# Kernel tuning notes

Measured on AMD Instinct MI355X. Metric: run time of the kernel, lower is better.

## Reference

```python
import jax, jax.numpy as jnp
import numpy as np


def setup_inputs() -> dict:
    key = jax.random.key(0)
    k1, _ = jax.random.split(key)
    x = jax.random.normal(k1, (32, 64, 192, 192), dtype=jnp.float32)
    gamma = jnp.zeros((1,), dtype=jnp.float32)
    return {"x": x, "gamma": gamma}


def reference(x, gamma):
    B, C, H, W = x.shape
    q = x.reshape(B, C, H * W)                      # [B, C, N]
    # energy[b, c, d] = <q[b,c,:], q[b,d,:]>
    energy = jnp.einsum('bcn,bdn->bcd', q, q)       # [B, C, C]
    # max-subtract trick: softmax over (max - energy)
    energy_new = jnp.max(energy, axis=-1, keepdims=True) - energy
    attention = jax.nn.softmax(energy_new, axis=-1)  # [B, C, C]
    out = jnp.einsum('bcd,bdn->bcn', attention, q)   # [B, C, N]
    out = out.reshape(B, C, H, W)
    return x * (gamma[0] * out) + x
```

## Files before the change

### kernel.cpp

```cpp
#include <hip/hip_runtime.h>


#define BATCH 32
#define CH 64
#define NSP 36864

#define KSPLIT 32
#define KPER (NSP / KSPLIT)
#define BK 128
#define SITER (KPER / BK)

#define NB 128
#define NCHUNK 4
#define NBLKY (NSP / (NB * NCHUNK))
#define XSTR 132

using frag  = __attribute__((ext_vector_type(8))) short;
using f32x4 = __attribute__((ext_vector_type(4))) float;

__device__ inline unsigned short f2bf(float f) {
    unsigned u = __builtin_bit_cast(unsigned, f);
    unsigned r = (u + 0x7FFFu + ((u >> 16) & 1u)) >> 16;
    return (unsigned short)r;
}
__device__ inline unsigned pack2(float a, float b) {
    return (unsigned)f2bf(a) | ((unsigned)f2bf(b) << 16);
}
__device__ inline int rotn(int c, int n) {
    return (n + (((c >> 3) & 3) << 4)) & (NB - 1);
}

__global__ __launch_bounds__(256, 4) void gram_kernel(const float* __restrict__ x,
                                                      float* __restrict__ part) {
    const int b = blockIdx.x;
    const int kb = blockIdx.y;
    const int tid = threadIdx.x;
    const int wv = tid >> 6;
    const int lane = tid & 63;
    const int l15 = lane & 15;
    const int quad = lane >> 4;

    __shared__ unsigned short tile[2][CH][BK + 8];

    const float* xb = x + (size_t)b * CH * NSP + (size_t)kb * KPER;

    f32x4 acc[4];
#pragma unroll
    for (int cb = 0; cb < 4; cb++)
#pragma unroll
        for (int r = 0; r < 4; r++) acc[cb][r] = 0.f;

    float4 v[8];
#pragma unroll
    for (int rep = 0; rep < 8; rep++) {
        int idx = rep * 256 + tid;
        int c = idx >> 5, kq = idx & 31;
        v[rep] = *(const float4*)&xb[(size_t)c * NSP + kq * 4];
    }

    int p = 0;
    for (int s = 0; s < SITER; s++) {
#pragma unroll
        for (int rep = 0; rep < 8; rep++) {
            int idx = rep * 256 + tid;
            int c = idx >> 5, kq = idx & 31;
            uint2 pp;
            pp.x = pack2(v[rep].x, v[rep].y);
            pp.y = pack2(v[rep].z, v[rep].w);
            *(uint2*)&tile[p][c][kq * 4] = pp;
        }
        __syncthreads();
        if (s + 1 < SITER) {
#pragma unroll
            for (int rep = 0; rep < 8; rep++) {
                int idx = rep * 256 + tid;
                int c = idx >> 5, kq = idx & 31;
                v[rep] = *(const float4*)&xb[(size_t)c * NSP + (s + 1) * BK + kq * 4];
            }
        }
#pragma unroll
        for (int ks = 0; ks < 4; ks++) {
            frag a = *(const frag*)&tile[p][wv * 16 + l15][ks * 32 + quad * 8];
#pragma unroll
            for (int cb = 0; cb < 4; cb++) {
                frag bb = *(const frag*)&tile[p][cb * 16 + l15][ks * 32 + quad * 8];
                acc[cb] = __builtin_amdgcn_mfma_f32_16x16x32_bf16(a, bb, acc[cb], 0, 0, 0);
            }
        }
        p ^= 1;
    }

    float* eb = part + ((size_t)kb * BATCH + b) * CH * CH;
#pragma unroll
    for (int cb = 0; cb < 4; cb++)
#pragma unroll
        for (int r = 0; r < 4; r++) {
            int row = wv * 16 + quad * 4 + r;
            int col = cb * 16 + l15;
            eb[row * CH + col] = acc[cb][r];
        }
}

__global__ __launch_bounds__(64) void softmax_kernel(const float* __restrict__ part,
                                                     float* __restrict__ att) {
    const int row = blockIdx.x;
    const int d = threadIdx.x;

    float e = 0.f;
#pragma unroll
    for (int kb = 0; kb < KSPLIT; kb++)
        e += part[(size_t)kb * (BATCH * CH * CH) + (size_t)row * CH + d];

    float m = e;
#pragma unroll
    for (int off = 32; off > 0; off >>= 1) m = fmaxf(m, __shfl_down(m, off));
    m = __shfl(m, 0);

    float en = m - e;

    float mx = en;
#pragma unroll
    for (int off = 32; off > 0; off >>= 1) mx = fmaxf(mx, __shfl_down(mx, off));
    mx = __shfl(mx, 0);

    float ex = __expf(en - mx);
    float s = ex;
#pragma unroll
    for (int off = 32; off > 0; off >>= 1) s += __shfl_down(s, off);
    s = __shfl(s, 0);

    att[(size_t)row * CH + d] = ex / s;
}

__global__ __launch_bounds__(256, 3) void proj_kernel(const float* __restrict__ x,
                                                      const float* __restrict__ att,
                                                      const float* __restrict__ gamma,
                                                      float* __restrict__ out) {
    const int b = blockIdx.x;
    const int tid = threadIdx.x;
    const int wv = tid >> 6;
    const int lane = tid & 63;
    const int l15 = lane & 15;
    const int quad = lane >> 4;

    __shared__ float xs[CH][XSTR];
    __shared__ unsigned short satt[CH][72];

    const float* xb = x + (size_t)b * CH * NSP;
    float* ob = out + (size_t)b * CH * NSP;

#pragma unroll
    for (int rep = 0; rep < 4; rep++) {
        int idx = rep * 256 + tid;
        int c = idx >> 4, j = idx & 15;
        float4 a4 = *(const float4*)&att[(size_t)b * CH * CH + c * CH + j * 4];
        uint2 pp;
        pp.x = pack2(a4.x, a4.y);
        pp.y = pack2(a4.z, a4.w);
        *(uint2*)&satt[c][j * 4] = pp;
    }

    const float g = gamma[0];
    const int nbase = blockIdx.y * (NB * NCHUNK);

    float4 v[8];
#pragma unroll
    for (int rep = 0; rep < 8; rep++) {
        int idx = rep * 256 + tid;
        int dd = idx >> 5, nq = idx & 31;
        v[rep] = *(const float4*)&xb[(size_t)dd * NSP + nbase + nq * 4];
    }

    for (int ch = 0; ch < NCHUNK; ch++) {
        const int n0 = nbase + ch * NB;

        __syncthreads();
#pragma unroll
        for (int rep = 0; rep < 8; rep++) {
            int idx = rep * 256 + tid;
            int dd = idx >> 5, nq = idx & 31;
            *(float4*)&xs[dd][rotn(dd, nq * 4)] = v[rep];
        }
        __syncthreads();

        if (ch + 1 < NCHUNK) {
#pragma unroll
            for (int rep = 0; rep < 8; rep++) {
                int idx = rep * 256 + tid;
                int dd = idx >> 5, nq = idx & 31;
                v[rep] = *(const float4*)&xb[(size_t)dd * NSP + n0 + NB + nq * 4];
            }
        }

        f32x4 acc[2][4];
#pragma unroll
        for (int t = 0; t < 2; t++)
#pragma unroll
            for (int cb = 0; cb < 4; cb++)
#pragma unroll
                for (int r = 0; r < 4; r++) acc[t][cb][r] = 0.f;

#pragma unroll
        for (int ks = 0; ks < 2; ks++) {
            frag af[4];
#pragma unroll
            for (int cb = 0; cb < 4; cb++)
                af[cb] = *(const frag*)&satt[cb * 16 + l15][ks * 32 + quad * 8];
#pragma unroll
            for (int t = 0; t < 2; t++) {
                int n = (wv * 2 + t) * 16 + l15;
                int k0 = ks * 32 + quad * 8;
                int np = (n + (quad << 4)) & (NB - 1);
                uint4 packed;
                packed.x = pack2(xs[k0 + 0][np], xs[k0 + 1][np]);
                packed.y = pack2(xs[k0 + 2][np], xs[k0 + 3][np]);
                packed.z = pack2(xs[k0 + 4][np], xs[k0 + 5][np]);
                packed.w = pack2(xs[k0 + 6][np], xs[k0 + 7][np]);
                frag bf = __builtin_bit_cast(frag, packed);
#pragma unroll
                for (int cb = 0; cb < 4; cb++)
                    acc[t][cb] = __builtin_amdgcn_mfma_f32_16x16x32_bf16(af[cb], bf, acc[t][cb], 0, 0, 0);
            }
        }

#pragma unroll
        for (int t = 0; t < 2; t++) {
            int n = (wv * 2 + t) * 16 + l15;
#pragma unroll
            for (int cb = 0; cb < 4; cb++)
#pragma unroll
                for (int r = 0; r < 4; r++) {
                    int c = cb * 16 + quad * 4 + r;
                    int np = rotn(c, n);
                    float xv = xs[c][np];
                    xs[c][np] = fmaf(xv * g, acc[t][cb][r], xv);
                }
        }
        __syncthreads();

#pragma unroll
        for (int rep = 0; rep < 8; rep++) {
            int idx = rep * 256 + tid;
            int dd = idx >> 5, nq = idx & 31;
            float4 r4 = *(const float4*)&xs[dd][rotn(dd, nq * 4)];
            *(float4*)&ob[(size_t)dd * NSP + n0 + nq * 4] = r4;
        }
    }
}

extern "C" void kernel_launch(void* const* d_in, const int* in_sizes, int n_in,
                              void* d_out, int out_size, void* d_ws, size_t ws_size,
                              hipStream_t stream) {
    const float* x = (const float*)d_in[0];
    const float* gamma = (const float*)d_in[1];
    float* out = (float*)d_out;

    float* part = (float*)d_ws;
    float* att = part + (size_t)KSPLIT * BATCH * CH * CH;

    gram_kernel<<<dim3(BATCH, KSPLIT), 256, 0, stream>>>(x, part);
    softmax_kernel<<<BATCH * CH, 64, 0, stream>>>(part, att);
    proj_kernel<<<dim3(BATCH, NBLKY), 256, 0, stream>>>(x, att, gamma, out);
}
```

Before: 687.1 us.

## Restructure proj to one tile per block, bf16 attention, retune gram split

The gram kernel now uses 48 K-splits with a 64-wide K tile and a higher occupancy hint. The softmax writes attention directly as bf16, so the projection kernel loads its A fragments straight from global memory with no LDS staging. The projection kernel drops the 4-chunk register-prefetch loop and handles one 128-column tile per block, launching 4x more blocks, and writes results straight to global rather than back through LDS. This trades explicit prefetch and coalesced float4 stores for more parallelism, with scattered scalar stores and more partial sums to reduce in softmax.

```diff
diff --git a/kernel.cpp b/kernel.cpp
--- a/kernel.cpp
+++ b/kernel.cpp
@@ -5,14 +5,13 @@
 #define CH 64
 #define NSP 36864
 
-#define KSPLIT 32
+#define KSPLIT 48
 #define KPER (NSP / KSPLIT)
-#define BK 128
+#define BK 64
 #define SITER (KPER / BK)
 
 #define NB 128
-#define NCHUNK 4
-#define NBLKY (NSP / (NB * NCHUNK))
+#define NBLKY (NSP / NB)
 #define XSTR 132
 
 using frag  = __attribute__((ext_vector_type(8))) short;
@@ -30,7 +29,7 @@
     return (n + (((c >> 3) & 3) << 4)) & (NB - 1);
 }
 
-__global__ __launch_bounds__(256, 4) void gram_kernel(const float* __restrict__ x,
+__global__ __launch_bounds__(256, 6) void gram_kernel(const float* __restrict__ x,
                                                       float* __restrict__ part) {
     const int b = blockIdx.x;
     const int kb = blockIdx.y;
@@ -50,20 +49,20 @@
 #pragma unroll
         for (int r = 0; r < 4; r++) acc[cb][r] = 0.f;
 
-    float4 v[8];
-#pragma unroll
-    for (int rep = 0; rep < 8; rep++) {
+    float4 v[4];
+#pragma unroll
+    for (int rep = 0; rep < 4; rep++) {
         int idx = rep * 256 + tid;
-        int c = idx >> 5, kq = idx & 31;
+        int c = idx >> 4, kq = idx & 15;
         v[rep] = *(const float4*)&xb[(size_t)c * NSP + kq * 4];
     }
 
     int p = 0;
     for (int s = 0; s < SITER; s++) {
 #pragma unroll
-        for (int rep = 0; rep < 8; rep++) {
+        for (int rep = 0; rep < 4; rep++) {
             int idx = rep * 256 + tid;
-            int c = idx >> 5, kq = idx & 31;
+            int c = idx >> 4, kq = idx & 15;
             uint2 pp;
             pp.x = pack2(v[rep].x, v[rep].y);
             pp.y = pack2(v[rep].z, v[rep].w);
@@ -72,14 +71,14 @@
         __syncthreads();
         if (s + 1 < SITER) {
 #pragma unroll
-            for (int rep = 0; rep < 8; rep++) {
+            for (int rep = 0; rep < 4; rep++) {
                 int idx = rep * 256 + tid;
-                int c = idx >> 5, kq = idx & 31;
+                int c = idx >> 4, kq = idx & 15;
                 v[rep] = *(const float4*)&xb[(size_t)c * NSP + (s + 1) * BK + kq * 4];
             }
         }
 #pragma unroll
-        for (int ks = 0; ks < 4; ks++) {
+        for (int ks = 0; ks < 2; ks++) {
             frag a = *(const frag*)&tile[p][wv * 16 + l15][ks * 32 + quad * 8];
 #pragma unroll
             for (int cb = 0; cb < 4; cb++) {
@@ -102,7 +101,7 @@
 }
 
 __global__ __launch_bounds__(64) void softmax_kernel(const float* __restrict__ part,
-                                                     float* __restrict__ att) {
+                                                     unsigned short* __restrict__ att_bf) {
     const int row = blockIdx.x;
     const int d = threadIdx.x;
 
@@ -129,14 +128,15 @@
     for (int off = 32; off > 0; off >>= 1) s += __shfl_down(s, off);
     s = __shfl(s, 0);
 
-    att[(size_t)row * CH + d] = ex / s;
-}
-
-__global__ __launch_bounds__(256, 3) void proj_kernel(const float* __restrict__ x,
-                                                      const float* __restrict__ att,
+    att_bf[(size_t)row * CH + d] = f2bf(ex / s);
+}
+
+__global__ __launch_bounds__(256, 4) void proj_kernel(const float* __restrict__ x,
+                                                      const unsigned short* __restrict__ att_bf,
                                                       const float* __restrict__ gamma,
                                                       float* __restrict__ out) {
     const int b = blockIdx.x;
+    const int n0 = blockIdx.y * NB;
     const int tid = threadIdx.x;
     const int wv = tid >> 6;
     const int lane = tid & 63;
@@ -144,107 +144,67 @@
     const int quad = lane >> 4;
 
     __shared__ float xs[CH][XSTR];
-    __shared__ unsigned short satt[CH][72];
 
     const float* xb = x + (size_t)b * CH * NSP;
     float* ob = out + (size_t)b * CH * NSP;
 
-#pragma unroll
-    for (int rep = 0; rep < 4; rep++) {
-        int idx = rep * 256 + tid;
-        int c = idx >> 4, j = idx & 15;
-        float4 a4 = *(const float4*)&att[(size_t)b * CH * CH + c * CH + j * 4];
-        uint2 pp;
-        pp.x = pack2(a4.x, a4.y);
-        pp.y = pack2(a4.z, a4.w);
-        *(uint2*)&satt[c][j * 4] = pp;
-    }
-
-    const float g = gamma[0];
-    const int nbase = blockIdx.y * (NB * NCHUNK);
-
-    float4 v[8];
+    frag af[2][4];
+#pragma unroll
+    for (int ks = 0; ks < 2; ks++)
+#pragma unroll
+        for (int cb = 0; cb < 4; cb++)
+            af[ks][cb] = *(const frag*)&att_bf[((size_t)b * CH + cb * 16 + l15) * CH
+                                               + ks * 32 + quad * 8];
+
 #pragma unroll
     for (int rep = 0; rep < 8; rep++) {
         int idx = rep * 256 + tid;
         int dd = idx >> 5, nq = idx & 31;
-        v[rep] = *(const float4*)&xb[(size_t)dd * NSP + nbase + nq * 4];
-    }
-
-    for (int ch = 0; ch < NCHUNK; ch++) {
-        const int n0 = nbase + ch * NB;
-
-        __syncthreads();
-#pragma unroll
-        for (int rep = 0; rep < 8; rep++) {
-            int idx = rep * 256 + tid;
-            int dd = idx >> 5, nq = idx & 31;
-            *(float4*)&xs[dd][rotn(dd, nq * 4)] = v[rep];
-        }
-        __syncthreads();
-
-        if (ch + 1 < NCHUNK) {
-#pragma unroll
-            for (int rep = 0; rep < 8; rep++) {
-                int idx = rep * 256 + tid;
-                int dd = idx >> 5, nq = idx & 31;
-                v[rep] = *(const float4*)&xb[(size_t)dd * NSP + n0 + NB + nq * 4];
-            }
-        }
-
-        f32x4 acc[2][4];
-#pragma unroll
-        for (int t = 0; t < 2; t++)
-#pragma unroll
-            for (int cb = 0; cb < 4; cb++)
-#pragma unroll
-                for (int r = 0; r < 4; r++) acc[t][cb][r] = 0.f;
-
-#pragma unroll
-        for (int ks = 0; ks < 2; ks++) {
-            frag af[4];
-#pragma unroll
-            for (int cb = 0; cb < 4; cb++)
-                af[cb] = *(const frag*)&satt[cb * 16 + l15][ks * 32 + quad * 8];
-#pragma unroll
-            for (int t = 0; t < 2; t++) {
-                int n = (wv * 2 + t) * 16 + l15;
-                int k0 = ks * 32 + quad * 8;
-                int np = (n + (quad << 4)) & (NB - 1);
-                uint4 packed;
-                packed.x = pack2(xs[k0 + 0][np], xs[k0 + 1][np]);
-                packed.y = pack2(xs[k0 + 2][np], xs[k0 + 3][np]);
-                packed.z = pack2(xs[k0 + 4][np], xs[k0 + 5][np]);
-                packed.w = pack2(xs[k0 + 6][np], xs[k0 + 7][np]);
-                frag bf = __builtin_bit_cast(frag, packed);
-#pragma unroll
-                for (int cb = 0; cb < 4; cb++)
-                    acc[t][cb] = __builtin_amdgcn_mfma_f32_16x16x32_bf16(af[cb], bf, acc[t][cb], 0, 0, 0);
-            }
-        }
-
+        float4 v = *(const float4*)&xb[(size_t)dd * NSP + n0 + nq * 4];
+        *(float4*)&xs[dd][rotn(dd, nq * 4)] = v;
+    }
+    __syncthreads();
+
+    const float g = gamma[0];
+
+    f32x4 acc[2][4];
+#pragma unroll
+    for (int t = 0; t < 2; t++)
+#pragma unroll
+        for (int cb = 0; cb < 4; cb++)
+#pragma unroll
+            for (int r = 0; r < 4; r++) acc[t][cb][r] = 0.f;
+
+#pragma unroll
+    for (int ks = 0; ks < 2; ks++) {
 #pragma unroll
         for (int t = 0; t < 2; t++) {
             int n = (wv * 2 + t) * 16 + l15;
+            int k0 = ks * 32 + quad * 8;
+            int np = (n + (quad << 4)) & (NB - 1);
+            uint4 packed;
+            packed.x = pack2(xs[k0 + 0][np], xs[k0 + 1][np]);
+            packed.y = pack2(xs[k0 + 2][np], xs[k0 + 3][np]);
+            packed.z = pack2(xs[k0 + 4][np], xs[k0 + 5][np]);
+            packed.w = pack2(xs[k0 + 6][np], xs[k0 + 7][np]);
+            frag bf = __builtin_bit_cast(frag, packed);
 #pragma unroll
             for (int cb = 0; cb < 4; cb++)
-#pragma unroll
-                for (int r = 0; r < 4; r++) {
-                    int c = cb * 16 + quad * 4 + r;
-                    int np = rotn(c, n);
-                    float xv = xs[c][np];
-                    xs[c][np] = fmaf(xv * g, acc[t][cb][r], xv);
-                }
-        }
-        __syncthreads();
-
-#pragma unroll
-        for (int rep = 0; rep < 8; rep++) {
-            int idx = rep * 256 + tid;
-            int dd = idx >> 5, nq = idx & 31;
-            float4 r4 = *(const float4*)&xs[dd][rotn(dd, nq * 4)];
-            *(float4*)&ob[(size_t)dd * NSP + n0 + nq * 4] = r4;
-        }
+                acc[t][cb] = __builtin_amdgcn_mfma_f32_16x16x32_bf16(af[ks][cb], bf, acc[t][cb], 0, 0, 0);
+        }
+    }
+
+#pragma unroll
+    for (int t = 0; t < 2; t++) {
+        int n = (wv * 2 + t) * 16 + l15;
+#pragma unroll
+        for (int cb = 0; cb < 4; cb++)
+#pragma unroll
+            for (int r = 0; r < 4; r++) {
+                int c = cb * 16 + quad * 4 + r;
+                float xv = xs[c][rotn(c, n)];
+                ob[(size_t)c * NSP + n0 + n] = fmaf(xv * g, acc[t][cb][r], xv);
+            }
     }
 }
 
@@ -256,9 +216,9 @@
     float* out = (float*)d_out;
 
     float* part = (float*)d_ws;
-    float* att = part + (size_t)KSPLIT * BATCH * CH * CH;
+    unsigned short* att_bf = (unsigned short*)(part + (size_t)KSPLIT * BATCH * CH * CH);
 
     gram_kernel<<<dim3(BATCH, KSPLIT), 256, 0, stream>>>(x, part);
-    softmax_kernel<<<BATCH * CH, 64, 0, stream>>>(part, att);
-    proj_kernel<<<dim3(BATCH, NBLKY), 256, 0, stream>>>(x, att, gamma, out);
-}
+    softmax_kernel<<<BATCH * CH, 64, 0, stream>>>(part, att_bf);
+    proj_kernel<<<dim3(BATCH, NBLKY), 256, 0, stream>>>(x, att_bf, gamma, out);
+}
```

New measurement: 598.9 us. -12.8%, faster.
